# Performance work log

Hardware: AMD Instinct MI355X
Metric: run time of the kernel (lower is better)

## Reference

```python
import jax, jax.numpy as jnp
import numpy as np

B, S, D, DS = 8, 2048, 1024, 128
TEMP = 1.0
C = 8.0


def setup_inputs() -> dict:
    key = jax.random.key(0)
    ks = jax.random.split(key, 8)
    s_in = 1.0 / np.sqrt(D)
    s_st = 1.0 / np.sqrt(DS)
    return {
        "x": jax.random.normal(ks[0], (B, S, D), jnp.float32),
        "W_k": jax.random.normal(ks[1], (DS, D), jnp.float32) * s_in,
        "W_v": jax.random.normal(ks[2], (DS, D), jnp.float32) * s_in,
        "W_q": jax.random.normal(ks[3], (DS, D), jnp.float32) * s_in,
        "W_alpha_w": jax.random.normal(ks[4], (DS, D), jnp.float32) * s_in,
        "W_alpha_b": jnp.zeros((DS,), jnp.float32),
        "lambda_param": jax.random.uniform(ks[5], (DS,), jnp.float32, 4.0, 9.0),
        "W_o": jax.random.normal(ks[6], (D, DS), jnp.float32) * s_st,
        "norm_weight": jnp.ones((DS,), jnp.float32),
    }


def _l2norm(z):
    # matches F.normalize(..., dim=-1) with eps=1e-12
    n = jnp.linalg.norm(z, axis=-1, keepdims=True)
    return z / jnp.maximum(n, 1e-12)


def reference(x, W_k, W_v, W_q, W_alpha_w, W_alpha_b, lambda_param, W_o, norm_weight):
    # projections
    k = _l2norm(x @ W_k.T)                      # [B,S,DS]
    v = x @ W_v.T                               # [B,S,DS]
    q = _l2norm(x @ W_q.T)                      # [B,S,DS]
    r = jax.nn.sigmoid(x @ W_alpha_w.T + W_alpha_b)
    log_a = jnp.log(jax.nn.sigmoid(lambda_param) + 1e-8)  # [DS]
    alpha = jnp.exp(C * r * log_a)              # [B,S,DS], data-dependent decay

    H0 = jnp.zeros((B, DS, DS), x.dtype)        # state indexed [b, k, v]

    def step(H, inp):
        k_t, v_t, q_t, a_t = inp                # each [B,DS]
        # surprise: prediction error against current state
        pred = jnp.einsum('bk,bkv->bv', q_t, H)
        err = jnp.sum((v_t - pred) ** 2, axis=-1, keepdims=True)  # [B,1]
        sur = jax.nn.sigmoid(err / (TEMP + 1e-6))                 # [B,1]
        # delta rule: k (x) v - k (x) (k^T H) = k (x) (v - k^T H)
        k_proj = jnp.einsum('bk,bkv->bv', k_t, H)
        delta = k_t[:, :, None] * (v_t - k_proj)[:, None, :]      # [B,DS,DS]
        a_e = a_t[:, :, None]                                     # decay on k-axis
        H = a_e * H + (1.0 - a_e) * (sur[:, :, None] * delta)
        y = jnp.einsum('bk,bkv->bv', q_t, H)
        return H, y

    seq = (k.transpose(1, 0, 2), v.transpose(1, 0, 2),
           q.transpose(1, 0, 2), alpha.transpose(1, 0, 2))
    _, ys = jax.lax.scan(step, H0, seq)         # ys: [S,B,DS]
    y = ys.transpose(1, 0, 2)                   # [B,S,DS]

    # RMSNorm (computed in fp32, like the torch module)
    yf = y.astype(jnp.float32)
    yn = yf * jax.lax.rsqrt(jnp.mean(yf * yf, axis=-1, keepdims=True) + 1e-6)
    yn = (yn * norm_weight).astype(y.dtype)
    return yn @ W_o.T                           # [B,S,D]
```

## Files before the change

kernel.cpp:

```cpp
#include <hip/hip_runtime.h>
#include <math.h>

#define S_LEN 2048
#define B_SZ 8
#define D_IN 1024
#define DS_ 128
#define INV_TEMP (1.0f/1.000001f)
#define LBUF 712

#define BAR_LDS() asm volatile("s_waitcnt lgkmcnt(0)\n\ts_barrier" ::: "memory")

#define DPPADD(x, ctrl) { int t_ = __builtin_amdgcn_update_dpp( \
    0, __float_as_int(x), ctrl, 0xF, 0xF, false); x += __int_as_float(t_); }
#define ROWSUM(x) { DPPADD(x, 0x128) DPPADD(x, 0x124) DPPADD(x, 0x122) DPPADD(x, 0x121) }
#define ROWSUM4(v4) { ROWSUM(v4.x) ROWSUM(v4.y) ROWSUM(v4.z) ROWSUM(v4.w) }

typedef unsigned int uint2v __attribute__((ext_vector_type(2)));
#define XSUM16(XV) { uint2v r_ = __builtin_amdgcn_permlane16_swap( \
    __float_as_uint(XV), __float_as_uint(XV), false, false); \
    XV = __uint_as_float(r_[0]) + __uint_as_float(r_[1]); }
#define XSUM32(XV) { uint2v r_ = __builtin_amdgcn_permlane32_swap( \
    __float_as_uint(XV), __float_as_uint(XV), false, false); \
    XV = __uint_as_float(r_[0]) + __uint_as_float(r_[1]); }

__global__ __launch_bounds__(256) void proj_gemm(
    const float* __restrict__ X,
    const float* __restrict__ Wk, const float* __restrict__ Wv,
    const float* __restrict__ Wq, const float* __restrict__ Wa,
    float* __restrict__ P)
{
    __shared__ __align__(16) float As[32][132];
    __shared__ __align__(16) float Bs[32][132];
    const int tid = threadIdx.x;
    const int m0 = blockIdx.x * 128;
    const int n0 = blockIdx.y * 128;
    const int sr = tid >> 3;
    const int sk = tid & 7;
    const float* Wbase = (n0 == 0) ? Wk : (n0 == 128) ? Wv : (n0 == 256) ? Wq : Wa;
    const int ty = tid >> 4, tx = tid & 15;

    float acc[8][8];
#pragma unroll
    for (int i = 0; i < 8; i++)
#pragma unroll
        for (int j = 0; j < 8; j++) acc[i][j] = 0.f;

    for (int k0 = 0; k0 < D_IN; k0 += 32) {
#pragma unroll
        for (int i = 0; i < 4; i++) {
            int m = sr + i * 32;
            float4 a4 = *(const float4*)(X + (size_t)(m0 + m) * D_IN + k0 + sk * 4);
            As[sk*4+0][m] = a4.x; As[sk*4+1][m] = a4.y;
            As[sk*4+2][m] = a4.z; As[sk*4+3][m] = a4.w;
            float4 b4 = *(const float4*)(Wbase + (size_t)m * D_IN + k0 + sk * 4);
            Bs[sk*4+0][m] = b4.x; Bs[sk*4+1][m] = b4.y;
            Bs[sk*4+2][m] = b4.z; Bs[sk*4+3][m] = b4.w;
        }
        __syncthreads();
#pragma unroll
        for (int kk = 0; kk < 32; kk++) {
            float4 a0 = *(const float4*)(&As[kk][ty * 8]);
            float4 a1 = *(const float4*)(&As[kk][ty * 8 + 4]);
            float4 b0 = *(const float4*)(&Bs[kk][tx * 8]);
            float4 b1 = *(const float4*)(&Bs[kk][tx * 8 + 4]);
            float a[8] = {a0.x,a0.y,a0.z,a0.w,a1.x,a1.y,a1.z,a1.w};
            float b[8] = {b0.x,b0.y,b0.z,b0.w,b1.x,b1.y,b1.z,b1.w};
#pragma unroll
            for (int i = 0; i < 8; i++)
#pragma unroll
                for (int j = 0; j < 8; j++)
                    acc[i][j] = fmaf(a[i], b[j], acc[i][j]);
        }
        __syncthreads();
    }
#pragma unroll
    for (int i = 0; i < 8; i++) {
        float4 o0; o0.x = acc[i][0]; o0.y = acc[i][1]; o0.z = acc[i][2]; o0.w = acc[i][3];
        float4 o1; o1.x = acc[i][4]; o1.y = acc[i][5]; o1.z = acc[i][6]; o1.w = acc[i][7];
        float* dst = P + (size_t)(m0 + ty * 8 + i) * 512 + n0 + tx * 8;
        *(float4*)(dst) = o0; *(float4*)(dst + 4) = o1;
    }
}

__global__ __launch_bounds__(128) void postproc(
    float* __restrict__ P, float* __restrict__ G,
    const float* __restrict__ bA, const float* __restrict__ lam)
{
    const int tok = blockIdx.x, i = threadIdx.x;
    float* row = P + (size_t)tok * 512;
    float kr = row[i], qr = row[256 + i], rr = row[384 + i];
    float ks = kr * kr, qs = qr * qr;
#pragma unroll
    for (int m = 1; m < 64; m <<= 1) { ks += __shfl_xor(ks, m); qs += __shfl_xor(qs, m); }
    __shared__ float sb[6];
    if ((i & 63) == 0) { sb[(i >> 6) * 2] = ks; sb[(i >> 6) * 2 + 1] = qs; }
    __syncthreads();
    float kinv = 1.0f / fmaxf(sqrtf(sb[0] + sb[2]), 1e-12f);
    float qinv = 1.0f / fmaxf(sqrtf(sb[1] + sb[3]), 1e-12f);
    float kn = kr * kinv, qn = qr * qinv;
    float sr = 1.0f / (1.0f + __expf(-(rr + bA[i])));
    float sl = 1.0f / (1.0f + __expf(-lam[i]));
    float la = logf(sl + 1e-8f);
    float al = __expf(8.0f * sr * la);
    row[i] = kn; row[256 + i] = qn; row[384 + i] = al;
    float gi = qn * (1.0f - al) * kn;
#pragma unroll
    for (int m = 1; m < 64; m <<= 1) gi += __shfl_xor(gi, m);
    if ((i & 63) == 0) sb[4 + (i >> 6)] = gi;
    __syncthreads();
    if (i == 0) G[tok] = sb[4] + sb[5];
}

__global__ __launch_bounds__(512, 2) void recurrence(
    const float* __restrict__ P, const float* __restrict__ G, float* __restrict__ Y)
{
    const int b = blockIdx.x;
    const int tid = threadIdx.x;
    const int c = tid & 15;
    const int vp = tid >> 4;
    const int wave = tid >> 6;
    const int co = c * 12;

    __shared__ __align__(16) float Pbuf[3][LBUF];
    __shared__ __align__(16) float errw[2][8];

    const float* Pb = P + (size_t)b * S_LEN * 512;
    const float* Gb = G + (size_t)b * S_LEN;
    float* Yb = Y + (size_t)b * S_LEN * DS_;

    float4 H0={0,0,0,0},H1={0,0,0,0},H2={0,0,0,0},H3={0,0,0,0},
           H4={0,0,0,0},H5={0,0,0,0},H6={0,0,0,0},H7={0,0,0,0};

    const bool isP = tid < 256;
    const bool isG = (tid == 256);
    int spos = 0;
    if (isP) {
        int i = tid * 2, s = i >> 7, idx = i & 127, cp = (idx >> 3) * 12 + (idx & 7);
        spos = (s == 0) ? cp : (s == 1) ? (576 + idx) : (s == 2) ? (192 + cp) : (384 + cp);
    }

    float2 rp0 = {0.f, 0.f}, rp1 = {0.f, 0.f};
    float rg0 = 0.f, rg1 = 0.f;
    if (isP) { rp0 = *(const float2*)(Pb + tid * 2); rp1 = *(const float2*)(Pb + 512 + tid * 2); }
    if (isG) { rg0 = Gb[0]; rg1 = Gb[1]; }
    if (isP) *(float2*)(&Pbuf[0][spos]) = rp0;
    if (isG) Pbuf[0][704] = rg0;
    __syncthreads();

#define DOTJ(qs, ks, zs, Hj) { \
    pr.x = fmaf(qs, Hj.x, pr.x); pr.y = fmaf(qs, Hj.y, pr.y); \
    pr.z = fmaf(qs, Hj.z, pr.z); pr.w = fmaf(qs, Hj.w, pr.w); \
    kp.x = fmaf(ks, Hj.x, kp.x); kp.y = fmaf(ks, Hj.y, kp.y); \
    kp.z = fmaf(ks, Hj.z, kp.z); kp.w = fmaf(ks, Hj.w, kp.w); \
    ya.x = fmaf(zs, Hj.x, ya.x); ya.y = fmaf(zs, Hj.y, ya.y); \
    ya.z = fmaf(zs, Hj.z, ya.z); ya.w = fmaf(zs, Hj.w, ya.w); }

#define UPDJ(as_, ws_, Hj) { \
    Hj.x = fmaf(as_, Hj.x, ws_ * sd.x); Hj.y = fmaf(as_, Hj.y, ws_ * sd.y); \
    Hj.z = fmaf(as_, Hj.z, ws_ * sd.z); Hj.w = fmaf(as_, Hj.w, ws_ * sd.w); }

#define STEP(T, PAR, RPS, RGS, RPL, RGL) { \
    float* cb = &Pbuf[(T) % 3][0]; \
    const float4 k0 = *(const float4*)(cb + co); \
    const float4 k1 = *(const float4*)(cb + co + 4); \
    const float4 q0 = *(const float4*)(cb + 192 + co); \
    const float4 q1 = *(const float4*)(cb + 192 + co + 4); \
    const float4 a0 = *(const float4*)(cb + 384 + co); \
    const float4 a1 = *(const float4*)(cb + 384 + co + 4); \
    const float4 vt = *(const float4*)(cb + 576 + vp * 4); \
    const float g = cb[704]; \
    float4 z0, z1, w0, w1; \
    z0.x = q0.x * a0.x; z0.y = q0.y * a0.y; z0.z = q0.z * a0.z; z0.w = q0.w * a0.w; \
    z1.x = q1.x * a1.x; z1.y = q1.y * a1.y; z1.z = q1.z * a1.z; z1.w = q1.w * a1.w; \
    w0.x = fmaf(-k0.x, a0.x, k0.x); w0.y = fmaf(-k0.y, a0.y, k0.y); \
    w0.z = fmaf(-k0.z, a0.z, k0.z); w0.w = fmaf(-k0.w, a0.w, k0.w); \
    w1.x = fmaf(-k1.x, a1.x, k1.x); w1.y = fmaf(-k1.y, a1.y, k1.y); \
    w1.z = fmaf(-k1.z, a1.z, k1.z); w1.w = fmaf(-k1.w, a1.w, k1.w); \
    float4 pr = {0,0,0,0}, kp = {0,0,0,0}, ya = {0,0,0,0}; \
    DOTJ(q0.x, k0.x, z0.x, H0) DOTJ(q0.y, k0.y, z0.y, H1) \
    DOTJ(q0.z, k0.z, z0.z, H2) DOTJ(q0.w, k0.w, z0.w, H3) \
    DOTJ(q1.x, k1.x, z1.x, H4) DOTJ(q1.y, k1.y, z1.y, H5) \
    DOTJ(q1.z, k1.z, z1.z, H6) DOTJ(q1.w, k1.w, z1.w, H7) \
    ROWSUM4(pr) ROWSUM4(kp) ROWSUM4(ya) \
    float4 d4; d4.x = vt.x - kp.x; d4.y = vt.y - kp.y; \
    d4.z = vt.z - kp.z; d4.w = vt.w - kp.w; \
    float ex = vt.x - pr.x, ey = vt.y - pr.y, ez = vt.z - pr.z, ew = vt.w - pr.w; \
    float ep = fmaf(ex, ex, fmaf(ey, ey, fmaf(ez, ez, ew * ew))); \
    XSUM16(ep) XSUM32(ep) \
    if ((tid & 63) == 0) errw[PAR][wave] = ep; \
    if ((T) + 1 < S_LEN) { \
        if (isP) *(float2*)(&Pbuf[((T) + 1) % 3][spos]) = RPS; \
        if (isG) Pbuf[((T) + 1) % 3][704] = RGS; } \
    if ((T) + 2 < S_LEN) { \
        if (isP) RPL = *(const float2*)(Pb + (size_t)((T) + 2) * 512 + tid * 2); \
        if (isG) RGL = Gb[(T) + 2]; } \
    BAR_LDS(); \
    const float4 ea = *(const float4*)(&errw[PAR][0]); \
    const float4 eb = *(const float4*)(&errw[PAR][4]); \
    float err = ((ea.x + ea.y) + (ea.z + ea.w)) + ((eb.x + eb.y) + (eb.z + eb.w)); \
    float sur = 1.0f / (1.0f + __expf(-err * INV_TEMP)); \
    float4 sd; sd.x = sur * d4.x; sd.y = sur * d4.y; \
    sd.z = sur * d4.z; sd.w = sur * d4.w; \
    if (c == 0) { \
        float sg = sur * g; float4 y4; \
        y4.x = fmaf(sg, d4.x, ya.x); y4.y = fmaf(sg, d4.y, ya.y); \
        y4.z = fmaf(sg, d4.z, ya.z); y4.w = fmaf(sg, d4.w, ya.w); \
        *(float4*)(Yb + (size_t)(T) * DS_ + vp * 4) = y4; } \
    UPDJ(a0.x, w0.x, H0) UPDJ(a0.y, w0.y, H1) \
    UPDJ(a0.z, w0.z, H2) UPDJ(a0.w, w0.w, H3) \
    UPDJ(a1.x, w1.x, H4) UPDJ(a1.y, w1.y, H5) \
    UPDJ(a1.z, w1.z, H6) UPDJ(a1.w, w1.w, H7) \
}

    for (int t = 0; t < S_LEN; t += 2) {
        STEP(t,     0, rp1, rg1, rp0, rg0)
        STEP(t + 1, 1, rp0, rg0, rp1, rg1)
    }
#undef DOTJ
#undef UPDJ
#undef STEP
}

__global__ __launch_bounds__(128) void rmsnorm(
    float* __restrict__ Y, const float* __restrict__ nw)
{
    const int tok = blockIdx.x, i = threadIdx.x;
    float y = Y[(size_t)tok * DS_ + i];
    float s = y * y;
#pragma unroll
    for (int m = 1; m < 64; m <<= 1) s += __shfl_xor(s, m);
    __shared__ float sb[2];
    if ((i & 63) == 0) sb[i >> 6] = s;
    __syncthreads();
    float ms = (sb[0] + sb[1]) * (1.0f / 128.0f);
    Y[(size_t)tok * DS_ + i] = y * rsqrtf(ms + 1e-6f) * nw[i];
}

__global__ __launch_bounds__(256) void out_gemm(
    const float* __restrict__ Yn, const float* __restrict__ Wo, float* __restrict__ Out)
{
    __shared__ __align__(16) float As[32][132];
    __shared__ __align__(16) float Bs[32][132];
    const int tid = threadIdx.x;
    const int m0 = blockIdx.x * 128;
    const int n0 = blockIdx.y * 128;
    const int sr = tid >> 3;
    const int sk = tid & 7;
    const int ty = tid >> 4, tx = tid & 15;

    float acc[8][8];
#pragma unroll
    for (int i = 0; i < 8; i++)
#pragma unroll
        for (int j = 0; j < 8; j++) acc[i][j] = 0.f;

    for (int k0 = 0; k0 < DS_; k0 += 32) {
#pragma unroll
        for (int i = 0; i < 4; i++) {
            int m = sr + i * 32;
            float4 a4 = *(const float4*)(Yn + (size_t)(m0 + m) * DS_ + k0 + sk * 4);
            As[sk*4+0][m] = a4.x; As[sk*4+1][m] = a4.y;
            As[sk*4+2][m] = a4.z; As[sk*4+3][m] = a4.w;
            float4 b4 = *(const float4*)(Wo + (size_t)(n0 + m) * DS_ + k0 + sk * 4);
            Bs[sk*4+0][m] = b4.x; Bs[sk*4+1][m] = b4.y;
            Bs[sk*4+2][m] = b4.z; Bs[sk*4+3][m] = b4.w;
        }
        __syncthreads();
#pragma unroll
        for (int kk = 0; kk < 32; kk++) {
            float4 a0 = *(const float4*)(&As[kk][ty * 8]);
            float4 a1 = *(const float4*)(&As[kk][ty * 8 + 4]);
            float4 b0 = *(const float4*)(&Bs[kk][tx * 8]);
            float4 b1 = *(const float4*)(&Bs[kk][tx * 8 + 4]);
            float a[8] = {a0.x,a0.y,a0.z,a0.w,a1.x,a1.y,a1.z,a1.w};
            float b[8] = {b0.x,b0.y,b0.z,b0.w,b1.x,b1.y,b1.z,b1.w};
#pragma unroll
            for (int i = 0; i < 8; i++)
#pragma unroll
                for (int j = 0; j < 8; j++)
                    acc[i][j] = fmaf(a[i], b[j], acc[i][j]);
        }
        __syncthreads();
    }
#pragma unroll
    for (int i = 0; i < 8; i++) {
        float4 o0; o0.x = acc[i][0]; o0.y = acc[i][1]; o0.z = acc[i][2]; o0.w = acc[i][3];
        float4 o1; o1.x = acc[i][4]; o1.y = acc[i][5]; o1.z = acc[i][6]; o1.w = acc[i][7];
        float* dst = Out + (size_t)(m0 + ty * 8 + i) * 1024 + n0 + tx * 8;
        *(float4*)(dst) = o0; *(float4*)(dst + 4) = o1;
    }
}

extern "C" void kernel_launch(void* const* d_in, const int* in_sizes, int n_in,
                              void* d_out, int out_size, void* d_ws, size_t ws_size,
                              hipStream_t stream)
{
    const float* x   = (const float*)d_in[0];
    const float* Wk  = (const float*)d_in[1];
    const float* Wv  = (const float*)d_in[2];
    const float* Wq  = (const float*)d_in[3];
    const float* Waw = (const float*)d_in[4];
    const float* Wab = (const float*)d_in[5];
    const float* lam = (const float*)d_in[6];
    const float* Wo  = (const float*)d_in[7];
    const float* nw  = (const float*)d_in[8];
    float* out = (float*)d_out;

    const size_t NTOK = (size_t)B_SZ * S_LEN;
    float* P  = (float*)d_ws;
    float* G  = P + NTOK * 512;
    float* Y  = G + NTOK;

    proj_gemm<<<dim3(NTOK / 128, 512 / 128), 256, 0, stream>>>(x, Wk, Wv, Wq, Waw, P);
    postproc<<<NTOK, 128, 0, stream>>>(P, G, Wab, lam);
    recurrence<<<B_SZ, 512, 0, stream>>>(P, G, Y);
    rmsnorm<<<NTOK, 128, 0, stream>>>(Y, nw);
    out_gemm<<<dim3(NTOK / 128, 1024 / 128), 256, 0, stream>>>(Y, Wo, out);
}
```

Measured before the change: 2.737 ms.

## Load per-step recurrence inputs directly from global into registers, drop LDS staging

The recurrence kernel no longer stages each token's k/q/alpha/v/g vectors through a triple-buffered LDS array. Each thread now loads its own slices straight from global memory into double-buffered registers, two steps ahead. This removes the LDS writes and reads and one synchronisation hazard per step. In exchange it adds redundant global/L2 loads, since many threads read the same k/q/alpha, and raises register pressure under a 512-thread, 2-block launch bound.

```diff
diff --git a/kernel.cpp b/kernel.cpp
--- a/kernel.cpp
+++ b/kernel.cpp
@@ -6,7 +6,6 @@
 #define D_IN 1024
 #define DS_ 128
 #define INV_TEMP (1.0f/1.000001f)
-#define LBUF 712
 
 #define BAR_LDS() asm volatile("s_waitcnt lgkmcnt(0)\n\ts_barrier" ::: "memory")
 
@@ -119,9 +118,9 @@
     const int c = tid & 15;
     const int vp = tid >> 4;
     const int wave = tid >> 6;
-    const int co = c * 12;
-
-    __shared__ __align__(16) float Pbuf[3][LBUF];
+    const int ko = c * 8;
+    const int vo = 128 + vp * 4;
+
     __shared__ __align__(16) float errw[2][8];
 
     const float* Pb = P + (size_t)b * S_LEN * 512;
@@ -131,21 +130,20 @@
     float4 H0={0,0,0,0},H1={0,0,0,0},H2={0,0,0,0},H3={0,0,0,0},
            H4={0,0,0,0},H5={0,0,0,0},H6={0,0,0,0},H7={0,0,0,0};
 
-    const bool isP = tid < 256;
-    const bool isG = (tid == 256);
-    int spos = 0;
-    if (isP) {
-        int i = tid * 2, s = i >> 7, idx = i & 127, cp = (idx >> 3) * 12 + (idx & 7);
-        spos = (s == 0) ? cp : (s == 1) ? (576 + idx) : (s == 2) ? (192 + cp) : (384 + cp);
-    }
-
-    float2 rp0 = {0.f, 0.f}, rp1 = {0.f, 0.f};
-    float rg0 = 0.f, rg1 = 0.f;
-    if (isP) { rp0 = *(const float2*)(Pb + tid * 2); rp1 = *(const float2*)(Pb + 512 + tid * 2); }
-    if (isG) { rg0 = Gb[0]; rg1 = Gb[1]; }
-    if (isP) *(float2*)(&Pbuf[0][spos]) = rp0;
-    if (isG) Pbuf[0][704] = rg0;
-    __syncthreads();
+    float4 kA0,kA1,qA0,qA1,aA0,aA1,vA; float gA;
+    float4 kB0,kB1,qB0,qB1,aB0,aB1,vB; float gB;
+    {
+        const float* p0 = Pb;
+        kA0 = *(const float4*)(p0 + ko);       kA1 = *(const float4*)(p0 + ko + 4);
+        qA0 = *(const float4*)(p0 + 256 + ko); qA1 = *(const float4*)(p0 + 256 + ko + 4);
+        aA0 = *(const float4*)(p0 + 384 + ko); aA1 = *(const float4*)(p0 + 384 + ko + 4);
+        vA  = *(const float4*)(p0 + vo);       gA  = Gb[0];
+        const float* p1 = Pb + 512;
+        kB0 = *(const float4*)(p1 + ko);       kB1 = *(const float4*)(p1 + ko + 4);
+        qB0 = *(const float4*)(p1 + 256 + ko); qB1 = *(const float4*)(p1 + 256 + ko + 4);
+        aB0 = *(const float4*)(p1 + 384 + ko); aB1 = *(const float4*)(p1 + 384 + ko + 4);
+        vB  = *(const float4*)(p1 + vo);       gB  = Gb[1];
+    }
 
 #define DOTJ(qs, ks, zs, Hj) { \
     pr.x = fmaf(qs, Hj.x, pr.x); pr.y = fmaf(qs, Hj.y, pr.y); \
@@ -159,41 +157,32 @@
     Hj.x = fmaf(as_, Hj.x, ws_ * sd.x); Hj.y = fmaf(as_, Hj.y, ws_ * sd.y); \
     Hj.z = fmaf(as_, Hj.z, ws_ * sd.z); Hj.w = fmaf(as_, Hj.w, ws_ * sd.w); }
 
-#define STEP(T, PAR, RPS, RGS, RPL, RGL) { \
-    float* cb = &Pbuf[(T) % 3][0]; \
-    const float4 k0 = *(const float4*)(cb + co); \
-    const float4 k1 = *(const float4*)(cb + co + 4); \
-    const float4 q0 = *(const float4*)(cb + 192 + co); \
-    const float4 q1 = *(const float4*)(cb + 192 + co + 4); \
-    const float4 a0 = *(const float4*)(cb + 384 + co); \
-    const float4 a1 = *(const float4*)(cb + 384 + co + 4); \
-    const float4 vt = *(const float4*)(cb + 576 + vp * 4); \
-    const float g = cb[704]; \
+#define STEP(T, PAR, K0,K1,Q0,Q1,A0,A1,VT,GS) { \
     float4 z0, z1, w0, w1; \
-    z0.x = q0.x * a0.x; z0.y = q0.y * a0.y; z0.z = q0.z * a0.z; z0.w = q0.w * a0.w; \
-    z1.x = q1.x * a1.x; z1.y = q1.y * a1.y; z1.z = q1.z * a1.z; z1.w = q1.w * a1.w; \
-    w0.x = fmaf(-k0.x, a0.x, k0.x); w0.y = fmaf(-k0.y, a0.y, k0.y); \
-    w0.z = fmaf(-k0.z, a0.z, k0.z); w0.w = fmaf(-k0.w, a0.w, k0.w); \
-    w1.x = fmaf(-k1.x, a1.x, k1.x); w1.y = fmaf(-k1.y, a1.y, k1.y); \
-    w1.z = fmaf(-k1.z, a1.z, k1.z); w1.w = fmaf(-k1.w, a1.w, k1.w); \
+    z0.x = Q0.x * A0.x; z0.y = Q0.y * A0.y; z0.z = Q0.z * A0.z; z0.w = Q0.w * A0.w; \
+    z1.x = Q1.x * A1.x; z1.y = Q1.y * A1.y; z1.z = Q1.z * A1.z; z1.w = Q1.w * A1.w; \
+    w0.x = fmaf(-K0.x, A0.x, K0.x); w0.y = fmaf(-K0.y, A0.y, K0.y); \
+    w0.z = fmaf(-K0.z, A0.z, K0.z); w0.w = fmaf(-K0.w, A0.w, K0.w); \
+    w1.x = fmaf(-K1.x, A1.x, K1.x); w1.y = fmaf(-K1.y, A1.y, K1.y); \
+    w1.z = fmaf(-K1.z, A1.z, K1.z); w1.w = fmaf(-K1.w, A1.w, K1.w); \
     float4 pr = {0,0,0,0}, kp = {0,0,0,0}, ya = {0,0,0,0}; \
-    DOTJ(q0.x, k0.x, z0.x, H0) DOTJ(q0.y, k0.y, z0.y, H1) \
-    DOTJ(q0.z, k0.z, z0.z, H2) DOTJ(q0.w, k0.w, z0.w, H3) \
-    DOTJ(q1.x, k1.x, z1.x, H4) DOTJ(q1.y, k1.y, z1.y, H5) \
-    DOTJ(q1.z, k1.z, z1.z, H6) DOTJ(q1.w, k1.w, z1.w, H7) \
+    DOTJ(Q0.x, K0.x, z0.x, H0) DOTJ(Q0.y, K0.y, z0.y, H1) \
+    DOTJ(Q0.z, K0.z, z0.z, H2) DOTJ(Q0.w, K0.w, z0.w, H3) \
+    DOTJ(Q1.x, K1.x, z1.x, H4) DOTJ(Q1.y, K1.y, z1.y, H5) \
+    DOTJ(Q1.z, K1.z, z1.z, H6) DOTJ(Q1.w, K1.w, z1.w, H7) \
     ROWSUM4(pr) ROWSUM4(kp) ROWSUM4(ya) \
-    float4 d4; d4.x = vt.x - kp.x; d4.y = vt.y - kp.y; \
-    d4.z = vt.z - kp.z; d4.w = vt.w - kp.w; \
-    float ex = vt.x - pr.x, ey = vt.y - pr.y, ez = vt.z - pr.z, ew = vt.w - pr.w; \
+    float4 d4; d4.x = VT.x - kp.x; d4.y = VT.y - kp.y; \
+    d4.z = VT.z - kp.z; d4.w = VT.w - kp.w; \
+    float ex = VT.x - pr.x, ey = VT.y - pr.y, ez = VT.z - pr.z, ew = VT.w - pr.w; \
     float ep = fmaf(ex, ex, fmaf(ey, ey, fmaf(ez, ez, ew * ew))); \
     XSUM16(ep) XSUM32(ep) \
     if ((tid & 63) == 0) errw[PAR][wave] = ep; \
-    if ((T) + 1 < S_LEN) { \
-        if (isP) *(float2*)(&Pbuf[((T) + 1) % 3][spos]) = RPS; \
-        if (isG) Pbuf[((T) + 1) % 3][704] = RGS; } \
+    const float gcur = GS; \
     if ((T) + 2 < S_LEN) { \
-        if (isP) RPL = *(const float2*)(Pb + (size_t)((T) + 2) * 512 + tid * 2); \
-        if (isG) RGL = Gb[(T) + 2]; } \
+        const float* ps_ = Pb + (size_t)((T) + 2) * 512; \
+        K0 = *(const float4*)(ps_ + ko);       K1 = *(const float4*)(ps_ + ko + 4); \
+        Q0 = *(const float4*)(ps_ + 256 + ko); Q1 = *(const float4*)(ps_ + 256 + ko + 4); \
+        VT = *(const float4*)(ps_ + vo); } \
     BAR_LDS(); \
     const float4 ea = *(const float4*)(&errw[PAR][0]); \
     const float4 eb = *(const float4*)(&errw[PAR][4]); \
@@ -202,19 +191,23 @@
     float4 sd; sd.x = sur * d4.x; sd.y = sur * d4.y; \
     sd.z = sur * d4.z; sd.w = sur * d4.w; \
     if (c == 0) { \
-        float sg = sur * g; float4 y4; \
+        float sg = sur * gcur; float4 y4; \
         y4.x = fmaf(sg, d4.x, ya.x); y4.y = fmaf(sg, d4.y, ya.y); \
         y4.z = fmaf(sg, d4.z, ya.z); y4.w = fmaf(sg, d4.w, ya.w); \
         *(float4*)(Yb + (size_t)(T) * DS_ + vp * 4) = y4; } \
-    UPDJ(a0.x, w0.x, H0) UPDJ(a0.y, w0.y, H1) \
-    UPDJ(a0.z, w0.z, H2) UPDJ(a0.w, w0.w, H3) \
-    UPDJ(a1.x, w1.x, H4) UPDJ(a1.y, w1.y, H5) \
-    UPDJ(a1.z, w1.z, H6) UPDJ(a1.w, w1.w, H7) \
+    if ((T) + 2 < S_LEN) GS = Gb[(T) + 2]; \
+    UPDJ(A0.x, w0.x, H0) UPDJ(A0.y, w0.y, H1) \
+    UPDJ(A0.z, w0.z, H2) UPDJ(A0.w, w0.w, H3) \
+    UPDJ(A1.x, w1.x, H4) UPDJ(A1.y, w1.y, H5) \
+    UPDJ(A1.z, w1.z, H6) UPDJ(A1.w, w1.w, H7) \
+    if ((T) + 2 < S_LEN) { \
+        const float* ps_ = Pb + (size_t)((T) + 2) * 512; \
+        A0 = *(const float4*)(ps_ + 384 + ko); A1 = *(const float4*)(ps_ + 384 + ko + 4); } \
 }
 
     for (int t = 0; t < S_LEN; t += 2) {
-        STEP(t,     0, rp1, rg1, rp0, rg0)
-        STEP(t + 1, 1, rp0, rg0, rp1, rg1)
+        STEP(t,     0, kA0,kA1,qA0,qA1,aA0,aA1,vA,gA)
+        STEP(t + 1, 1, kB0,kB1,qB0,qB1,aB0,aB1,vB,gB)
     }
 #undef DOTJ
 #undef UPDJ
```

New measurement: 2.744 ms. No clear change (+0.2%).
